# Performance work log

Hardware: AMD Instinct MI355X
Metric: run time of the kernel (lower is better)

Reference implementation:

```python
import jax, jax.numpy as jnp
import numpy as np

BATCH, INPUT_DIM, HIDDEN_DIM, SEQ_LENGTH = 128, 256, 512, 1024


def setup_inputs() -> dict:
    key = jax.random.key(0)
    k1, k2, k3, k4, k5 = jax.random.split(key, 5)
    s = 1.0 / np.sqrt(HIDDEN_DIM)  # PyTorch GRU init: U(-1/sqrt(H), 1/sqrt(H))
    return {
        "input_features": jax.random.normal(k1, (BATCH, INPUT_DIM), dtype=jnp.float32),
        # PyTorch layout: rows stacked as [reset; update; new], each [H, *]
        "w_ih": jax.random.uniform(k2, (3 * HIDDEN_DIM, INPUT_DIM), minval=-s, maxval=s, dtype=jnp.float32),
        "w_hh": jax.random.uniform(k3, (3 * HIDDEN_DIM, HIDDEN_DIM), minval=-s, maxval=s, dtype=jnp.float32),
        "b_ih": jax.random.uniform(k4, (3 * HIDDEN_DIM,), minval=-s, maxval=s, dtype=jnp.float32),
        "b_hh": jax.random.uniform(k5, (3 * HIDDEN_DIM,), minval=-s, maxval=s, dtype=jnp.float32),
    }


def reference(input_features, w_ih, w_hh, b_ih, b_hh):
    # Decoder: run the GRU cell SEQ_LENGTH times with the SAME input x each
    # step, feeding back the hidden state; collect per-step outputs.
    B = input_features.shape[0]
    H = w_hh.shape[1]
    # Input contribution is constant across steps -> compute once.  [B, 3H]
    gi = input_features @ w_ih.T + b_ih
    gi_r, gi_z, gi_n = jnp.split(gi, 3, axis=-1)

    def step(h, _):
        gh = h @ w_hh.T + b_hh  # [B, 3H]
        gh_r, gh_z, gh_n = jnp.split(gh, 3, axis=-1)
        r = jax.nn.sigmoid(gi_r + gh_r)
        z = jax.nn.sigmoid(gi_z + gh_z)
        n = jnp.tanh(gi_n + r * gh_n)
        h_new = (1.0 - z) * n + z * h
        return h_new, h_new

    h0 = jnp.zeros((B, H), dtype=input_features.dtype)
    _, outs = jax.lax.scan(step, h0, None, length=SEQ_LENGTH)  # [S, B, H]
    return jnp.transpose(outs, (1, 0, 2))  # [B, SEQ_LENGTH, H]
```

## Files before the change

kernel.cpp:

```cpp
#include <hip/hip_runtime.h>
#include <hip/hip_bf16.h>
#include <stdint.h>


constexpr int SEQ = 1024;
constexpr int BATCH = 128;
constexpr int IND = 256;
constexpr int HD = 512;
constexpr int BG = 8;
constexpr int HG = 32;
constexpr int ROWS = BATCH / BG;
constexpr int NT = 3;

using frag16 = __attribute__((ext_vector_type(8))) short;
using f32x4  = __attribute__((ext_vector_type(4))) float;

constexpr size_t WS_HBUF  = 0;
constexpr size_t WS_FLAGS = (size_t)2 * BATCH * HD * 2;

__device__ __forceinline__ float sigmoid_f(float x) {
    return 1.f / (1.f + __expf(-x));
}
__device__ __forceinline__ float tanh_f(float x) {
    float e = __expf(2.f * x);
    return 1.f - 2.f / (e + 1.f);
}
__device__ __forceinline__ short f2bf(float x) {
    return (short)__bfloat16_as_ushort(__float2bfloat16(x));
}

__global__ __launch_bounds__(64) void gru_kernel(
    const float* __restrict__ x,
    const float* __restrict__ w_ih,
    const float* __restrict__ w_hh,
    const float* __restrict__ b_ih,
    const float* __restrict__ b_hh,
    unsigned* __restrict__ hbuf_u32,
    unsigned* __restrict__ flags,
    float* __restrict__ out)
{
    const int lane = threadIdx.x;
    const int bg = blockIdx.x & 7;
    const int hg = blockIdx.x >> 3;
    const int b0 = bg * ROWS;
    const int c0 = hg * 16;
    const int nlo = lane & 15;
    const int quad = lane >> 4;

    int gcol[NT];
    gcol[0] = c0 + nlo;
    gcol[1] = HD + c0 + nlo;
    gcol[2] = 2 * HD + c0 + nlo;

    __shared__ frag16 ldsB[NT * 16 * 64];
#pragma unroll
    for (int t = 0; t < NT; ++t) {
        for (int kc = 0; kc < 16; ++kc) {
            const float* src = w_hh + (size_t)gcol[t] * HD + kc * 32 + quad * 8;
            float4 v0 = *(const float4*)src;
            float4 v1 = *(const float4*)(src + 4);
            frag16 f;
            f[0] = f2bf(v0.x); f[1] = f2bf(v0.y); f[2] = f2bf(v0.z); f[3] = f2bf(v0.w);
            f[4] = f2bf(v1.x); f[5] = f2bf(v1.y); f[6] = f2bf(v1.z); f[7] = f2bf(v1.w);
            ldsB[(t * 16 + kc) * 64 + lane] = f;
        }
    }

    float gi[NT][4];
    float bhn = b_hh[gcol[2]];
#pragma unroll
    for (int t = 0; t < NT; ++t) {
        float bi = b_ih[gcol[t]] + ((t < 2) ? b_hh[gcol[t]] : 0.f);
#pragma unroll
        for (int r = 0; r < 4; ++r) gi[t][r] = bi;
    }
    for (int r = 0; r < 4; ++r) {
        const float4* xr = (const float4*)(x + (size_t)(b0 + quad * 4 + r) * IND);
        for (int kc = 0; kc < IND / 4; ++kc) {
            float4 xv = xr[kc];
#pragma unroll
            for (int t = 0; t < NT; ++t) {
                float4 wv = ((const float4*)(w_ih + (size_t)gcol[t] * IND))[kc];
                gi[t][r] += xv.x * wv.x + xv.y * wv.y + xv.z * wv.z + xv.w * wv.w;
            }
        }
    }

    const int HWORDS = BATCH * HD / 2;
    const uint64_t a_dw = ((uint64_t)(b0 + nlo) * HD + quad * 8) >> 1;

    float hreg[4];
#pragma unroll
    for (int r = 0; r < 4; ++r) hreg[r] = 0.f;

    unsigned* myflag = flags + bg * HG + hg;
    unsigned* pollflag = flags + bg * HG + (lane & 31);

    for (int s = 0; s < SEQ; ++s) {
        f32x4 C[NT];
#pragma unroll
        for (int t = 0; t < NT; ++t) C[t] = (f32x4){0.f, 0.f, 0.f, 0.f};

        if (s > 0) {
            unsigned long long* hb =
                (unsigned long long*)(hbuf_u32 + (s & 1) * HWORDS);
            unsigned long long a0[16], a1[16];
#pragma unroll
            for (int kc = 0; kc < 16; ++kc) {
                unsigned long long* p = hb + ((a_dw + kc * 16) >> 1);
                a0[kc] = __hip_atomic_load(p,     __ATOMIC_RELAXED, __HIP_MEMORY_SCOPE_SYSTEM);
                a1[kc] = __hip_atomic_load(p + 1, __ATOMIC_RELAXED, __HIP_MEMORY_SCOPE_SYSTEM);
            }
#pragma unroll
            for (int kc = 0; kc < 16; ++kc) {
                union { unsigned long long u[2]; frag16 f; } af;
                af.u[0] = a0[kc];
                af.u[1] = a1[kc];
#pragma unroll
                for (int t = 0; t < NT; ++t) {
                    frag16 bfr = ldsB[(t * 16 + kc) * 64 + lane];
                    C[t] = __builtin_amdgcn_mfma_f32_16x16x32_bf16(af.f, bfr, C[t], 0, 0, 0);
                }
            }
        }

        unsigned* hw = hbuf_u32 + ((s + 1) & 1) * HWORDS;
#pragma unroll
        for (int r = 0; r < 4; ++r) {
            float gr  = gi[0][r] + C[0][r];
            float gz  = gi[1][r] + C[1][r];
            float ghn = C[2][r] + bhn;
            float rr = sigmoid_f(gr);
            float zz = sigmoid_f(gz);
            float nn = tanh_f(gi[2][r] + rr * ghn);
            float hn = (1.f - zz) * nn + zz * hreg[r];
            hreg[r] = hn;
            int row = b0 + quad * 4 + r;
            int col = c0 + nlo;
            out[(uint64_t)row * (SEQ * HD) + (uint64_t)s * HD + col] = hn;
            unsigned own = (unsigned)(unsigned short)f2bf(hn);
            unsigned other = (unsigned)__shfl_xor((int)own, 1);
            if ((lane & 1) == 0) {
                unsigned dw = own | (other << 16);
                __hip_atomic_store(hw + ((unsigned)(row * HD + col) >> 1), dw,
                                   __ATOMIC_RELAXED, __HIP_MEMORY_SCOPE_SYSTEM);
            }
        }

        if (s < SEQ - 1) {
            asm volatile("s_waitcnt vmcnt(0)" ::: "memory");
            if (lane == 0)
                __hip_atomic_store(myflag, (unsigned)(s + 1),
                                   __ATOMIC_RELAXED, __HIP_MEMORY_SCOPE_SYSTEM);
            bool done = false;
            do {
                unsigned v = __hip_atomic_load(pollflag, __ATOMIC_RELAXED,
                                               __HIP_MEMORY_SCOPE_SYSTEM);
                done = (__ballot(v > (unsigned)s) == ~0ull);
            } while (!done);
            asm volatile("" ::: "memory");
        }
    }
}

extern "C" void kernel_launch(void* const* d_in, const int* in_sizes, int n_in,
                              void* d_out, int out_size, void* d_ws, size_t ws_size,
                              hipStream_t stream) {
    (void)in_sizes; (void)n_in; (void)out_size; (void)ws_size;
    const float* x    = (const float*)d_in[0];
    const float* w_ih = (const float*)d_in[1];
    const float* w_hh = (const float*)d_in[2];
    const float* b_ih = (const float*)d_in[3];
    const float* b_hh = (const float*)d_in[4];

    char* ws = (char*)d_ws;
    unsigned* hbuf  = (unsigned*)(ws + WS_HBUF);
    unsigned* flags = (unsigned*)(ws + WS_FLAGS);

    hipMemsetAsync(flags, 0, (size_t)BG * HG * sizeof(unsigned), stream);
    gru_kernel<<<BG * HG, 64, 0, stream>>>(x, w_ih, w_hh, b_ih, b_hh, hbuf, flags,
                                           (float*)d_out);
}
```

Measured before the change: 3.306 ms.

## Replace flag barrier with sentinel-polled output buffer for cross-block h exchange

Drops the separate bf16 h exchange buffer and the per-step flag store and poll. The output is prefilled with 0xFF (NaN, bit 30 set), and each block polls the previous step's fp32 outputs directly until no word still carries the sentinel, then converts them to bf16 for the MFMA. New h is clamped to [-1,1], so bit 30 is never set in valid data. This removes the flag round trip and the separate store, but adds a 256MB memset and doubles the bytes read per poll.

```diff
diff --git a/kernel.cpp b/kernel.cpp
--- a/kernel.cpp
+++ b/kernel.cpp
@@ -15,9 +15,6 @@
 using frag16 = __attribute__((ext_vector_type(8))) short;
 using f32x4  = __attribute__((ext_vector_type(4))) float;
 
-constexpr size_t WS_HBUF  = 0;
-constexpr size_t WS_FLAGS = (size_t)2 * BATCH * HD * 2;
-
 __device__ __forceinline__ float sigmoid_f(float x) {
     return 1.f / (1.f + __expf(-x));
 }
@@ -29,14 +26,12 @@
     return (short)__bfloat16_as_ushort(__float2bfloat16(x));
 }
 
-__global__ __launch_bounds__(64) void gru_kernel(
+__global__ __launch_bounds__(64, 1) void gru_kernel(
     const float* __restrict__ x,
     const float* __restrict__ w_ih,
     const float* __restrict__ w_hh,
     const float* __restrict__ b_ih,
     const float* __restrict__ b_hh,
-    unsigned* __restrict__ hbuf_u32,
-    unsigned* __restrict__ flags,
     float* __restrict__ out)
 {
     const int lane = threadIdx.x;
@@ -86,15 +81,11 @@
         }
     }
 
-    const int HWORDS = BATCH * HD / 2;
-    const uint64_t a_dw = ((uint64_t)(b0 + nlo) * HD + quad * 8) >> 1;
+    const float* pbase = out + (size_t)(b0 + nlo) * (SEQ * HD) + quad * 8;
 
     float hreg[4];
 #pragma unroll
     for (int r = 0; r < 4; ++r) hreg[r] = 0.f;
-
-    unsigned* myflag = flags + bg * HG + hg;
-    unsigned* pollflag = flags + bg * HG + (lane & 31);
 
     for (int s = 0; s < SEQ; ++s) {
         f32x4 C[NT];
@@ -102,29 +93,45 @@
         for (int t = 0; t < NT; ++t) C[t] = (f32x4){0.f, 0.f, 0.f, 0.f};
 
         if (s > 0) {
-            unsigned long long* hb =
-                (unsigned long long*)(hbuf_u32 + (s & 1) * HWORDS);
-            unsigned long long a0[16], a1[16];
+            const float* hrow = pbase + (size_t)(s - 1) * HD;
+            f32x4 raw[32];
+            for (int tries = 0;; ++tries) {
+                if (tries) __builtin_amdgcn_s_sleep(2);
 #pragma unroll
-            for (int kc = 0; kc < 16; ++kc) {
-                unsigned long long* p = hb + ((a_dw + kc * 16) >> 1);
-                a0[kc] = __hip_atomic_load(p,     __ATOMIC_RELAXED, __HIP_MEMORY_SCOPE_SYSTEM);
-                a1[kc] = __hip_atomic_load(p + 1, __ATOMIC_RELAXED, __HIP_MEMORY_SCOPE_SYSTEM);
+                for (int kc = 0; kc < 16; ++kc) {
+                    asm volatile("global_load_dwordx4 %0, %1, off sc0 sc1"
+                                 : "=v"(raw[2 * kc])
+                                 : "v"(hrow + kc * 32) : "memory");
+                    asm volatile("global_load_dwordx4 %0, %1, off sc0 sc1"
+                                 : "=v"(raw[2 * kc + 1])
+                                 : "v"(hrow + kc * 32 + 4) : "memory");
+                }
+                asm volatile("s_waitcnt vmcnt(0)" ::: "memory");
+                __builtin_amdgcn_sched_barrier(0);
+                unsigned orr = 0u;
+#pragma unroll
+                for (int i = 0; i < 32; ++i) {
+                    orr |= __float_as_uint(raw[i][0]) | __float_as_uint(raw[i][1]) |
+                           __float_as_uint(raw[i][2]) | __float_as_uint(raw[i][3]);
+                }
+                if (__ballot(((orr >> 30) & 1u) == 0u) == ~0ull) break;
             }
 #pragma unroll
             for (int kc = 0; kc < 16; ++kc) {
-                union { unsigned long long u[2]; frag16 f; } af;
-                af.u[0] = a0[kc];
-                af.u[1] = a1[kc];
+                frag16 af;
+#pragma unroll
+                for (int j = 0; j < 4; ++j) {
+                    af[j]     = f2bf(raw[2 * kc][j]);
+                    af[j + 4] = f2bf(raw[2 * kc + 1][j]);
+                }
 #pragma unroll
                 for (int t = 0; t < NT; ++t) {
                     frag16 bfr = ldsB[(t * 16 + kc) * 64 + lane];
-                    C[t] = __builtin_amdgcn_mfma_f32_16x16x32_bf16(af.f, bfr, C[t], 0, 0, 0);
+                    C[t] = __builtin_amdgcn_mfma_f32_16x16x32_bf16(af, bfr, C[t], 0, 0, 0);
                 }
             }
         }
 
-        unsigned* hw = hbuf_u32 + ((s + 1) & 1) * HWORDS;
 #pragma unroll
         for (int r = 0; r < 4; ++r) {
             float gr  = gi[0][r] + C[0][r];
@@ -134,31 +141,13 @@
             float zz = sigmoid_f(gz);
             float nn = tanh_f(gi[2][r] + rr * ghn);
             float hn = (1.f - zz) * nn + zz * hreg[r];
+            hn = fminf(1.f, fmaxf(-1.f, hn));
             hreg[r] = hn;
             int row = b0 + quad * 4 + r;
-            int col = c0 + nlo;
-            out[(uint64_t)row * (SEQ * HD) + (uint64_t)s * HD + col] = hn;
-            unsigned own = (unsigned)(unsigned short)f2bf(hn);
-            unsigned other = (unsigned)__shfl_xor((int)own, 1);
-            if ((lane & 1) == 0) {
-                unsigned dw = own | (other << 16);
-                __hip_atomic_store(hw + ((unsigned)(row * HD + col) >> 1), dw,
-                                   __ATOMIC_RELAXED, __HIP_MEMORY_SCOPE_SYSTEM);
-            }
-        }
-
-        if (s < SEQ - 1) {
-            asm volatile("s_waitcnt vmcnt(0)" ::: "memory");
-            if (lane == 0)
-                __hip_atomic_store(myflag, (unsigned)(s + 1),
-                                   __ATOMIC_RELAXED, __HIP_MEMORY_SCOPE_SYSTEM);
-            bool done = false;
-            do {
-                unsigned v = __hip_atomic_load(pollflag, __ATOMIC_RELAXED,
-                                               __HIP_MEMORY_SCOPE_SYSTEM);
-                done = (__ballot(v > (unsigned)s) == ~0ull);
-            } while (!done);
-            asm volatile("" ::: "memory");
+            unsigned* dst = (unsigned*)out + (size_t)row * (SEQ * HD) +
+                            (size_t)s * HD + (c0 + nlo);
+            __hip_atomic_store(dst, __float_as_uint(hn),
+                               __ATOMIC_RELAXED, __HIP_MEMORY_SCOPE_SYSTEM);
         }
     }
 }
@@ -166,18 +155,13 @@
 extern "C" void kernel_launch(void* const* d_in, const int* in_sizes, int n_in,
                               void* d_out, int out_size, void* d_ws, size_t ws_size,
                               hipStream_t stream) {
-    (void)in_sizes; (void)n_in; (void)out_size; (void)ws_size;
+    (void)in_sizes; (void)n_in; (void)out_size; (void)d_ws; (void)ws_size;
     const float* x    = (const float*)d_in[0];
     const float* w_ih = (const float*)d_in[1];
     const float* w_hh = (const float*)d_in[2];
     const float* b_ih = (const float*)d_in[3];
     const float* b_hh = (const float*)d_in[4];
 
-    char* ws = (char*)d_ws;
-    unsigned* hbuf  = (unsigned*)(ws + WS_HBUF);
-    unsigned* flags = (unsigned*)(ws + WS_FLAGS);
-
-    hipMemsetAsync(flags, 0, (size_t)BG * HG * sizeof(unsigned), stream);
-    gru_kernel<<<BG * HG, 64, 0, stream>>>(x, w_ih, w_hh, b_ih, b_hh, hbuf, flags,
-                                           (float*)d_out);
+    hipMemsetAsync(d_out, 0xFF, (size_t)BATCH * SEQ * HD * sizeof(float), stream);
+    gru_kernel<<<BG * HG, 64, 0, stream>>>(x, w_ih, w_hh, b_ih, b_hh, (float*)d_out);
 }
```

Result: slower. 4.762 ms (+44.0%).
